# Kernel optimization log

Hardware: AMD Instinct MI355X
Metric: run time of the kernel (lower is better)

The kernel has to match this reference:

```python
import jax, jax.numpy as jnp
import numpy as np

B, M, N, DQ, H = 4, 4096, 4096, 256, 64

def setup_inputs() -> dict:
    key = jax.random.key(0)
    k1, k2, k3, k4 = jax.random.split(key, 4)
    x = jax.random.normal(k1, (B, M, DQ), dtype=jnp.float32)
    cond = jax.random.normal(k2, (B, N, DQ), dtype=jnp.float32)
    Wq = jax.random.normal(k3, (DQ, H), dtype=jnp.float32) * (1.0 / np.sqrt(DQ))
    Wkv = jax.random.normal(k4, (DQ, 2 * H), dtype=jnp.float32) * (1.0 / np.sqrt(DQ))
    return {"x": x, "cond": cond, "Wq": Wq, "Wkv": Wkv}

def reference(x, cond, Wq, Wkv):
    h = Wq.shape[1]
    q = jnp.einsum('bmi,ih->bmh', x, Wq)          # [B,M,H]
    kv = jnp.einsum('bni,ih->bnh', cond, Wkv)     # [B,N,2H]
    k, v = jnp.split(kv, 2, axis=-1)              # each [B,N,H]
    qk = jnp.einsum('bmd,bnd->bmn', q, k) / jnp.sqrt(jnp.asarray(h, q.dtype))
    attn = jax.nn.softmax(qk, axis=-1)            # [B,M,N]
    out = jnp.einsum('bmn,bnd->bmd', attn, v)     # [B,M,H]
    return out
```

## Files before the change

kernel.cpp:

```cpp
#include <hip/hip_runtime.h>
#include <hip/hip_bf16.h>
#include <cstdint>


#define BB 4
#define MM 4096
#define NN 4096
#define DQm 256
#define DH 64
#define NSP 8
#define NITER (NN / 64 / NSP)
#define QSCALE 0.18033688011112042f

typedef _Float16 half8 __attribute__((ext_vector_type(8)));
typedef _Float16 half4 __attribute__((ext_vector_type(4)));
typedef float floatx16 __attribute__((ext_vector_type(16)));

static __device__ __forceinline__ unsigned pkrtz(float a, float b) {
    union { __fp16 h __attribute__((ext_vector_type(2))); unsigned u; } cv;
    cv.h = __builtin_amdgcn_cvt_pkrtz(a, b);
    return cv.u;
}

__global__ __launch_bounds__(256) void wtrans_kernel(const float* __restrict__ Wq,
                                                     const float* __restrict__ Wkv,
                                                     _Float16* __restrict__ wt) {
    int cout = blockIdx.x;
    int t = threadIdx.x;
    float v = (cout < 64) ? Wq[t * 64 + cout] * QSCALE : Wkv[t * 128 + (cout - 64)];
    _Float16 hi = (_Float16)v;
    _Float16 lo = (_Float16)(v - (float)hi);
    wt[cout * DQm + t] = hi;
    wt[192 * DQm + cout * DQm + t] = lo;
}

__global__ __launch_bounds__(256) void proj_kernel(const float* __restrict__ x,
                                                   const float* __restrict__ cond,
                                                   const _Float16* __restrict__ wt,
                                                   _Float16* __restrict__ q_h,
                                                   _Float16* __restrict__ k_h,
                                                   _Float16* __restrict__ vt_h) {
    __shared__ __align__(16) _Float16 xh[64][264];
    __shared__ __align__(16) _Float16 xl[64][264];
    const int t = threadIdx.x;
    const bool isq = blockIdx.x < (BB * MM / 64);
    const int blk = isq ? blockIdx.x : blockIdx.x - BB * MM / 64;
    const long row0 = (long)blk * 64;
    const float4* xg = (const float4*)((isq ? x : cond) + row0 * DQm);
#pragma unroll
    for (int it = 0; it < 16; ++it) {
        int fid = t + it * 256;
        int row = fid >> 6, c4 = fid & 63;
        float4 v = xg[fid];
        half4 hh = {(_Float16)v.x, (_Float16)v.y, (_Float16)v.z, (_Float16)v.w};
        half4 hl = {(_Float16)(v.x - (float)hh[0]), (_Float16)(v.y - (float)hh[1]),
                    (_Float16)(v.z - (float)hh[2]), (_Float16)(v.w - (float)hh[3])};
        *(half4*)(&xh[row][c4 * 4]) = hh;
        *(half4*)(&xl[row][c4 * 4]) = hl;
    }
    __syncthreads();
    const int lane = t & 63, w = t >> 6, c = lane & 31, h = lane >> 5;
    const _Float16* wlo = wt + 192 * DQm;

    if (isq) {
        const int rt = w & 1, ct = w >> 1;
        floatx16 a1, a2, a3;
#pragma unroll
        for (int i = 0; i < 16; ++i) { a1[i] = 0.f; a2[i] = 0.f; a3[i] = 0.f; }
#pragma unroll
        for (int kt = 0; kt < 16; ++kt) {
            half8 ah = *(const half8*)(&xh[rt * 32 + c][kt * 16 + h * 8]);
            half8 al = *(const half8*)(&xl[rt * 32 + c][kt * 16 + h * 8]);
            half8 bh = *(const half8*)(wt  + (long)(ct * 32 + c) * DQm + kt * 16 + h * 8);
            half8 bl = *(const half8*)(wlo + (long)(ct * 32 + c) * DQm + kt * 16 + h * 8);
            a1 = __builtin_amdgcn_mfma_f32_32x32x16_f16(ah, bh, a1, 0, 0, 0);
            a2 = __builtin_amdgcn_mfma_f32_32x32x16_f16(ah, bl, a2, 0, 0, 0);
            a3 = __builtin_amdgcn_mfma_f32_32x32x16_f16(al, bh, a3, 0, 0, 0);
        }
#pragma unroll
        for (int r = 0; r < 16; ++r) {
            int m = (r & 3) + 8 * (r >> 2) + 4 * h;
            q_h[(row0 + rt * 32 + m) * DH + ct * 32 + c] = (_Float16)(a1[r] + a2[r] + a3[r]);
        }
    } else {
        const int rt = w & 1, ctp = w >> 1;
        floatx16 a1[2], a2[2], a3[2];
#pragma unroll
        for (int i = 0; i < 16; ++i) {
            a1[0][i] = 0.f; a2[0][i] = 0.f; a3[0][i] = 0.f;
            a1[1][i] = 0.f; a2[1][i] = 0.f; a3[1][i] = 0.f;
        }
#pragma unroll
        for (int kt = 0; kt < 16; ++kt) {
            half8 ah = *(const half8*)(&xh[rt * 32 + c][kt * 16 + h * 8]);
            half8 al = *(const half8*)(&xl[rt * 32 + c][kt * 16 + h * 8]);
#pragma unroll
            for (int i = 0; i < 2; ++i) {
                long wrow = 64 + (ctp * 2 + i) * 32 + c;
                half8 bh = *(const half8*)(wt  + wrow * DQm + kt * 16 + h * 8);
                half8 bl = *(const half8*)(wlo + wrow * DQm + kt * 16 + h * 8);
                a1[i] = __builtin_amdgcn_mfma_f32_32x32x16_f16(ah, bh, a1[i], 0, 0, 0);
                a2[i] = __builtin_amdgcn_mfma_f32_32x32x16_f16(ah, bl, a2[i], 0, 0, 0);
                a3[i] = __builtin_amdgcn_mfma_f32_32x32x16_f16(al, bh, a3[i], 0, 0, 0);
            }
        }
#pragma unroll
        for (int i = 0; i < 2; ++i) {
            int cout = (ctp * 2 + i) * 32 + c;
            if (cout < 64) {
#pragma unroll
                for (int r = 0; r < 16; ++r) {
                    int m = (r & 3) + 8 * (r >> 2) + 4 * h;
                    k_h[(row0 + rt * 32 + m) * DH + cout] =
                        (_Float16)(a1[i][r] + a2[i][r] + a3[i][r]);
                }
            } else {
                int d = cout - 64;
                long bb = row0 >> 12;
#pragma unroll
                for (int s2 = 0; s2 < 4; ++s2) {
                    long n = row0 + rt * 32 + 8 * s2 + 4 * h;
                    half4 hv;
#pragma unroll
                    for (int j = 0; j < 4; ++j)
                        hv[j] = (_Float16)(a1[i][s2 * 4 + j] + a2[i][s2 * 4 + j] +
                                           a3[i][s2 * 4 + j]);
                    *(half4*)(vt_h + (bb * DH + d) * NN + (n & 4095)) = hv;
                }
            }
        }
    }
}

__global__ __launch_bounds__(256, 4) void fa_kernel(const _Float16* __restrict__ q_h,
                                                    const _Float16* __restrict__ k_h,
                                                    const _Float16* __restrict__ vt_h,
                                                    float* __restrict__ Opart,
                                                    float2* __restrict__ ml) {
    __shared__ __align__(16) _Float16 k_lds[64][72];
    __shared__ __align__(16) _Float16 vt_lds[64][72];

    const int t = threadIdx.x;
    const int w = t >> 6;
    const int lane = t & 63;
    const int c = lane & 31;
    const int h = lane >> 5;

    const int bid = blockIdx.x;
    const int sp = bid >> 7;
    const int b  = (bid >> 5) & 3;
    const int mt = bid & 31;
    const int mbase = mt * 128 + w * 32;
    const long qrow = (long)b * MM + mbase + c;

    half8 qf[4];
#pragma unroll
    for (int kt = 0; kt < 4; ++kt)
        qf[kt] = *(const half8*)(q_h + qrow * DH + kt * 16 + h * 8);

    floatx16 Oc0, Oc1;
#pragma unroll
    for (int i = 0; i < 16; ++i) { Oc0[i] = 0.f; Oc1[i] = 0.f; }
    float m_run = 8.0f, l_run = 0.f;

#pragma unroll 1
    for (int nt = sp * NITER; nt < sp * NITER + NITER; ++nt) {
        const int n0 = nt * 64;
        __syncthreads();
        {
            const uint4* kg = (const uint4*)(k_h + ((long)b * NN + n0) * DH);
#pragma unroll
            for (int it = 0; it < 2; ++it) {
                int cid = t + it * 256;
                int r = cid >> 3, q = cid & 7;
                *(uint4*)(&k_lds[r][q * 8]) = kg[cid];
                *(uint4*)(&vt_lds[r][q * 8]) =
                    *(const uint4*)(vt_h + ((long)b * DH + r) * NN + n0 + q * 8);
            }
        }
        __syncthreads();

        floatx16 Sc[2];
        __builtin_amdgcn_s_setprio(1);
#pragma unroll
        for (int a = 0; a < 2; ++a) {
            floatx16 acc;
#pragma unroll
            for (int i = 0; i < 16; ++i) acc[i] = 0.f;
#pragma unroll
            for (int kt = 0; kt < 4; ++kt) {
                half8 af = *(const half8*)(&k_lds[a * 32 + c][kt * 16 + h * 8]);
                acc = __builtin_amdgcn_mfma_f32_32x32x16_f16(af, qf[kt], acc, 0, 0, 0);
            }
            Sc[a] = acc;
        }
        __builtin_amdgcn_s_setprio(0);

        float t8v[8];
#pragma unroll
        for (int i = 0; i < 8; ++i)
            t8v[i] = fmaxf(fmaxf(Sc[0][2 * i], Sc[0][2 * i + 1]),
                           fmaxf(Sc[1][2 * i], Sc[1][2 * i + 1]));
        float ta = fmaxf(fmaxf(t8v[0], t8v[1]), t8v[2]);
        float tb = fmaxf(fmaxf(t8v[3], t8v[4]), t8v[5]);
        float tmax = fmaxf(fmaxf(ta, tb), fmaxf(t8v[6], t8v[7]));
        tmax = fmaxf(tmax, __shfl_xor(tmax, 32, 64));
        if (__any(tmax > m_run + 8.0f)) {
            float m_new = fmaxf(m_run, tmax);
            float alpha = exp2f(m_run - m_new);
            l_run *= alpha;
#pragma unroll
            for (int i = 0; i < 16; ++i) { Oc0[i] *= alpha; Oc1[i] *= alpha; }
            m_run = m_new;
        }
#pragma unroll
        for (int a = 0; a < 2; ++a)
#pragma unroll
            for (int r = 0; r < 16; ++r) Sc[a][r] = exp2f(Sc[a][r] - m_run);

        {
            float ts[16];
#pragma unroll
            for (int i = 0; i < 16; ++i) ts[i] = Sc[0][i] + Sc[1][i];
#pragma unroll
            for (int i = 0; i < 8; ++i) ts[i] += ts[i + 8];
#pragma unroll
            for (int i = 0; i < 4; ++i) ts[i] += ts[i + 4];
            ts[0] += ts[2]; ts[1] += ts[3];
            float tsum = ts[0] + ts[1];
            tsum += __shfl_xor(tsum, 32, 64);
            l_run += tsum;
        }

#pragma unroll
        for (int a = 0; a < 2; ++a) {
            uint2 pk0 = {pkrtz(Sc[a][0],  Sc[a][1]),  pkrtz(Sc[a][2],  Sc[a][3])};
            uint2 pk1 = {pkrtz(Sc[a][4],  Sc[a][5]),  pkrtz(Sc[a][6],  Sc[a][7])};
            uint2 pk2 = {pkrtz(Sc[a][8],  Sc[a][9]),  pkrtz(Sc[a][10], Sc[a][11])};
            uint2 pk3 = {pkrtz(Sc[a][12], Sc[a][13]), pkrtz(Sc[a][14], Sc[a][15])};
            union { uint4 u; half8 f; } f0, f1;
#if __has_builtin(__builtin_amdgcn_permlane32_swap)
            {
                auto r0s = __builtin_amdgcn_permlane32_swap(pk0.x, pk1.x, false, false);
                auto r1s = __builtin_amdgcn_permlane32_swap(pk0.y, pk1.y, false, false);
                auto r2s = __builtin_amdgcn_permlane32_swap(pk2.x, pk3.x, false, false);
                auto r3s = __builtin_amdgcn_permlane32_swap(pk2.y, pk3.y, false, false);
                f0.u.x = r0s[0]; f0.u.z = r0s[1];
                f0.u.y = r1s[0]; f0.u.w = r1s[1];
                f1.u.x = r2s[0]; f1.u.z = r2s[1];
                f1.u.y = r3s[0]; f1.u.w = r3s[1];
            }
#else
            {
                uint2 s0, s1, ex0, ex1;
                s0.x = h ? pk0.x : pk1.x;  s0.y = h ? pk0.y : pk1.y;
                s1.x = h ? pk2.x : pk3.x;  s1.y = h ? pk2.y : pk3.y;
                ex0.x = __shfl_xor((int)s0.x, 32, 64);
                ex0.y = __shfl_xor((int)s0.y, 32, 64);
                ex1.x = __shfl_xor((int)s1.x, 32, 64);
                ex1.y = __shfl_xor((int)s1.y, 32, 64);
                f0.u.x = h ? ex0.x : pk0.x;  f0.u.y = h ? ex0.y : pk0.y;
                f0.u.z = h ? pk1.x : ex0.x;  f0.u.w = h ? pk1.y : ex0.y;
                f1.u.x = h ? ex1.x : pk2.x;  f1.u.y = h ? ex1.y : pk2.y;
                f1.u.z = h ? pk3.x : ex1.x;  f1.u.w = h ? pk3.y : ex1.y;
            }
#endif
            __builtin_amdgcn_s_setprio(1);
#pragma unroll
            for (int bq = 0; bq < 2; ++bq) {
                int kt = 2 * a + bq;
                half8 pf = bq ? f1.f : f0.f;
                half8 vf0 = *(const half8*)(&vt_lds[c][kt * 16 + h * 8]);
                half8 vf1 = *(const half8*)(&vt_lds[32 + c][kt * 16 + h * 8]);
                Oc0 = __builtin_amdgcn_mfma_f32_32x32x16_f16(vf0, pf, Oc0, 0, 0, 0);
                Oc1 = __builtin_amdgcn_mfma_f32_32x32x16_f16(vf1, pf, Oc1, 0, 0, 0);
            }
            __builtin_amdgcn_s_setprio(0);
        }
    }

    const long obase = ((long)sp * BB * MM + (long)b * MM + mbase + c) * DH;
#pragma unroll
    for (int dt = 0; dt < 2; ++dt) {
        const floatx16& O = dt ? Oc1 : Oc0;
#pragma unroll
        for (int s2 = 0; s2 < 4; ++s2) {
            float4 v;
            v.x = O[s2 * 4 + 0]; v.y = O[s2 * 4 + 1];
            v.z = O[s2 * 4 + 2]; v.w = O[s2 * 4 + 3];
            *(float4*)(Opart + obase + dt * 32 + s2 * 8 + h * 4) = v;
        }
    }
    if (h == 0)
        ml[((long)sp * BB + b) * MM + mbase + c] = make_float2(m_run, l_run);
}

__global__ __launch_bounds__(256) void merge_kernel(const float* __restrict__ Opart,
                                                    const float2* __restrict__ ml,
                                                    float* __restrict__ out) {
    const long g4 = (long)blockIdx.x * 256 + threadIdx.x;
    const long row = g4 >> 4;
    float2 p[NSP];
    float mmax = -INFINITY;
#pragma unroll
    for (int i = 0; i < NSP; ++i) {
        p[i] = ml[(long)i * BB * MM + row];
        mmax = fmaxf(mmax, p[i].x);
    }
    float denom = 0.f;
    float4 o = make_float4(0.f, 0.f, 0.f, 0.f);
    const float4* Op4 = (const float4*)Opart;
#pragma unroll
    for (int i = 0; i < NSP; ++i) {
        float ai = exp2f(p[i].x - mmax);
        denom += ai * p[i].y;
        float4 v = Op4[(long)i * (BB * MM * DH / 4) + g4];
        o.x += ai * v.x; o.y += ai * v.y; o.z += ai * v.z; o.w += ai * v.w;
    }
    float inv = 1.0f / denom;
    o.x *= inv; o.y *= inv; o.z *= inv; o.w *= inv;
    ((float4*)out)[g4] = o;
}

extern "C" void kernel_launch(void* const* d_in, const int* in_sizes, int n_in,
                              void* d_out, int out_size, void* d_ws, size_t ws_size,
                              hipStream_t stream) {
    const float* x    = (const float*)d_in[0];
    const float* cond = (const float*)d_in[1];
    const float* Wq   = (const float*)d_in[2];
    const float* Wkv  = (const float*)d_in[3];
    float* out = (float*)d_out;

    char* ws = (char*)d_ws;
    _Float16* wt   = (_Float16*)(ws);
    _Float16* q_h  = (_Float16*)(ws + 196608);
    _Float16* k_h  = (_Float16*)(ws + 196608 + 2097152);
    _Float16* vt_h = (_Float16*)(ws + 196608 + 2 * 2097152);
    float*    Op   = (float*)(ws + 196608 + 3 * 2097152);
    float2*   mlp  = (float2*)(ws + 196608 + 3 * 2097152 + (size_t)NSP * 4194304);

    wtrans_kernel<<<192, 256, 0, stream>>>(Wq, Wkv, wt);
    proj_kernel<<<BB * (MM + NN) / 64, 256, 0, stream>>>(x, cond, wt, q_h, k_h, vt_h);
    fa_kernel<<<NSP * BB * 32, 256, 0, stream>>>(q_h, k_h, vt_h, Op, mlp);
    merge_kernel<<<BB * MM * DH / 4 / 256, 256, 0, stream>>>(Op, mlp, out);
}
```

Measured before the change: 133.2 us.

## Double-buffer K/V tiles with direct global-to-LDS loads and XOR swizzle

Replaces the register-staged K and V^T tile loads in the attention kernel with global_load_lds direct-to-LDS transfers into a double buffer. The next tile is prefetched while the current one is processed, and one barrier per iteration replaces two. The padded LDS layout becomes an XOR-swizzled 64-column layout to avoid bank conflicts without padding. This doubles LDS use per block, which may affect occupancy. Correctness relies on the barrier and vmcnt semantics of global_load_lds, since there is no explicit wait before the tile is read.

```diff
diff --git a/kernel.cpp b/kernel.cpp
--- a/kernel.cpp
+++ b/kernel.cpp
@@ -20,6 +20,12 @@
     union { __fp16 h __attribute__((ext_vector_type(2))); unsigned u; } cv;
     cv.h = __builtin_amdgcn_cvt_pkrtz(a, b);
     return cv.u;
+}
+
+static __device__ __forceinline__ void gload16(const void* g, void* l) {
+    __builtin_amdgcn_global_load_lds(
+        (const __attribute__((address_space(1))) void*)g,
+        (__attribute__((address_space(3))) void*)l, 16, 0, 0);
 }
 
 __global__ __launch_bounds__(256) void wtrans_kernel(const float* __restrict__ Wq,
@@ -137,8 +143,8 @@
                                                     const _Float16* __restrict__ vt_h,
                                                     float* __restrict__ Opart,
                                                     float2* __restrict__ ml) {
-    __shared__ __align__(16) _Float16 k_lds[64][72];
-    __shared__ __align__(16) _Float16 vt_lds[64][72];
+    __shared__ __align__(16) _Float16 k_lds[2][64][64];
+    __shared__ __align__(16) _Float16 vt_lds[2][64][64];
 
     const int t = threadIdx.x;
     const int w = t >> 6;
@@ -153,6 +159,35 @@
     const int mbase = mt * 128 + w * 32;
     const long qrow = (long)b * MM + mbase + c;
 
+    const int p0 = w * 2048 + (lane << 4);
+    const int p1 = p0 + 1024;
+    const int q0 = p0 ^ (((p0 >> 7) & 7) << 4);
+    const int q1 = p1 ^ (((p1 >> 7) & 7) << 4);
+    const int n0f = sp * NITER * 64;
+    const char* ks0 = (const char*)k_h + ((long)b * NN + n0f) * DH * 2 + q0;
+    const char* ks1 = (const char*)k_h + ((long)b * NN + n0f) * DH * 2 + q1;
+    const char* vs0 = (const char*)vt_h +
+                      (((long)b * DH + (p0 >> 7)) * NN + n0f) * 2 + (q0 & 127);
+    const char* vs1 = (const char*)vt_h +
+                      (((long)b * DH + (p1 >> 7)) * NN + n0f) * 2 + (q1 & 127);
+
+#define STAGE(bufi)                                                   \
+    do {                                                              \
+        char* kld = (char*)(&k_lds[bufi][0][0]) + w * 2048;           \
+        char* vld = (char*)(&vt_lds[bufi][0][0]) + w * 2048;          \
+        gload16(ks0, kld);                                            \
+        gload16(ks1, kld + 1024);                                     \
+        gload16(vs0, vld);                                            \
+        gload16(vs1, vld + 1024);                                     \
+        ks0 += 64 * DH * 2; ks1 += 64 * DH * 2;                       \
+        vs0 += 128; vs1 += 128;                                       \
+    } while (0)
+
+    const int swb = (c & 7) << 4;
+    int koff[4];
+#pragma unroll
+    for (int kt = 0; kt < 4; ++kt) koff[kt] = (kt * 32 + h * 16) ^ swb;
+
     half8 qf[4];
 #pragma unroll
     for (int kt = 0; kt < 4; ++kt)
@@ -163,22 +198,16 @@
     for (int i = 0; i < 16; ++i) { Oc0[i] = 0.f; Oc1[i] = 0.f; }
     float m_run = 8.0f, l_run = 0.f;
 
+    STAGE(0);
+    __syncthreads();
+
 #pragma unroll 1
-    for (int nt = sp * NITER; nt < sp * NITER + NITER; ++nt) {
-        const int n0 = nt * 64;
-        __syncthreads();
-        {
-            const uint4* kg = (const uint4*)(k_h + ((long)b * NN + n0) * DH);
-#pragma unroll
-            for (int it = 0; it < 2; ++it) {
-                int cid = t + it * 256;
-                int r = cid >> 3, q = cid & 7;
-                *(uint4*)(&k_lds[r][q * 8]) = kg[cid];
-                *(uint4*)(&vt_lds[r][q * 8]) =
-                    *(const uint4*)(vt_h + ((long)b * DH + r) * NN + n0 + q * 8);
-            }
-        }
-        __syncthreads();
+    for (int it = 0; it < NITER; ++it) {
+        const int pb = it & 1;
+        if (it + 1 < NITER) STAGE(pb ^ 1);
+
+        const char* kbase = (const char*)(&k_lds[pb][0][0]);
+        const char* vbase = (const char*)(&vt_lds[pb][0][0]);
 
         floatx16 Sc[2];
         __builtin_amdgcn_s_setprio(1);
@@ -189,7 +218,7 @@
             for (int i = 0; i < 16; ++i) acc[i] = 0.f;
 #pragma unroll
             for (int kt = 0; kt < 4; ++kt) {
-                half8 af = *(const half8*)(&k_lds[a * 32 + c][kt * 16 + h * 8]);
+                half8 af = *(const half8*)(kbase + (a * 32 + c) * 128 + koff[kt]);
                 acc = __builtin_amdgcn_mfma_f32_32x32x16_f16(af, qf[kt], acc, 0, 0, 0);
             }
             Sc[a] = acc;
@@ -270,14 +299,17 @@
             for (int bq = 0; bq < 2; ++bq) {
                 int kt = 2 * a + bq;
                 half8 pf = bq ? f1.f : f0.f;
-                half8 vf0 = *(const half8*)(&vt_lds[c][kt * 16 + h * 8]);
-                half8 vf1 = *(const half8*)(&vt_lds[32 + c][kt * 16 + h * 8]);
+                half8 vf0 = *(const half8*)(vbase + c * 128 + koff[kt]);
+                half8 vf1 = *(const half8*)(vbase + (32 + c) * 128 + koff[kt]);
                 Oc0 = __builtin_amdgcn_mfma_f32_32x32x16_f16(vf0, pf, Oc0, 0, 0, 0);
                 Oc1 = __builtin_amdgcn_mfma_f32_32x32x16_f16(vf1, pf, Oc1, 0, 0, 0);
             }
             __builtin_amdgcn_s_setprio(0);
         }
-    }
+
+        __syncthreads();
+    }
+#undef STAGE
 
     const long obase = ((long)sp * BB * MM + (long)b * MM + mbase + c) * DH;
 #pragma unroll
```

Result: no change. 134.9 us (+1.2%).
